# Optimization experiments

Hardware: AMD Instinct MI355X
Metric: run time of the kernel (lower is better)

Reference implementation:

```python
import jax, jax.numpy as jnp
import numpy as np

N_NODES = 100000
N_EDGES = 3200000
IN_FEATS = 512
HIDDEN = 64
N_CLASSES = 32


def setup_inputs() -> dict:
    key = jax.random.key(0)
    k1, k2, k3, k4 = jax.random.split(key, 4)
    x = jax.random.normal(k1, (N_NODES, IN_FEATS), dtype=jnp.float32)
    edge_index = jax.random.randint(k2, (2, N_EDGES), 0, N_NODES, dtype=jnp.int64)
    # Glorot-ish init for weights
    W1 = jax.random.normal(k3, (IN_FEATS, HIDDEN), dtype=jnp.float32) / np.sqrt(IN_FEATS)
    b1 = jnp.zeros((HIDDEN,), dtype=jnp.float32)
    W2 = jax.random.normal(k4, (HIDDEN, N_CLASSES), dtype=jnp.float32) / np.sqrt(HIDDEN)
    b2 = jnp.zeros((N_CLASSES,), dtype=jnp.float32)
    return {"x": x, "edge_index": edge_index, "W1": W1, "b1": b1, "W2": W2, "b2": b2}


def reference(x, edge_index, W1, b1, W2, b2):
    N = x.shape[0]
    # GCNConv default: add self-loops, unit edge weights (edge_attr is None for Cora)
    loop = jnp.arange(N, dtype=edge_index.dtype)
    src = jnp.concatenate([edge_index[0], loop])  # [E+N]
    dst = jnp.concatenate([edge_index[1], loop])  # [E+N]
    w = jnp.ones(src.shape[0], dtype=x.dtype)
    # symmetric normalization: deg^-1/2[src] * w * deg^-1/2[dst]
    deg = jax.ops.segment_sum(w, dst, num_segments=N)
    dinv = jnp.where(deg > 0, jax.lax.rsqrt(deg), 0.0)
    norm = dinv[src] * w * dinv[dst]  # [E+N]

    def gcn_layer(h, W, b):
        h = h @ W                              # transform first (out dim small)
        msg = h[src] * norm[:, None]           # gather + scale  [E+N, d_out]
        agg = jax.ops.segment_sum(msg, dst, num_segments=N)  # scatter-add
        return agg + b

    h = jax.nn.relu(gcn_layer(x, W1, b1))
    # F.dropout(training=self.training) -> identity in eval mode
    out = gcn_layer(h, W2, b2)
    return jax.nn.log_softmax(out, axis=1)
```

## Files before the change

### kernel.cpp

```cpp
#include <hip/hip_runtime.h>
#include <hip/hip_fp16.h>
#include <math.h>

constexpr int N_NODES = 100000;
constexpr int N_EDGES = 3200000;
constexpr int IN_F = 512;
constexpr int HID = 64;
constexpr int NCLS = 32;
constexpr int CAP = 80;
constexpr int SHIFT = 9;
constexpr int NB = 196;
constexpr int BCAPC = 16976;
constexpr int CHUNK = 8192;
constexpr int SENT = N_NODES;

constexpr int GEMM1_BLOCKS = (N_NODES + 63) / 64;
constexpr int PART_BLOCKS  = (N_EDGES + CHUNK - 1) / CHUNK;

typedef short short8 __attribute__((ext_vector_type(8)));
typedef float f32x4 __attribute__((ext_vector_type(4)));
typedef int intx4 __attribute__((ext_vector_type(4)));

__device__ __forceinline__ unsigned short f2bf(float f) {
    union { float f; unsigned int u; } v; v.f = f;
    unsigned int r = (v.u + 0x7fffu + ((v.u >> 16) & 1u)) >> 16;
    return (unsigned short)r;
}
__device__ __forceinline__ float bf2f(unsigned short h) {
    union { unsigned int u; float f; } v; v.u = ((unsigned int)h) << 16;
    return v.f;
}
__device__ __forceinline__ unsigned char f2e5(float f) {
    unsigned short u = __half_as_ushort(__float2half(f));
    return (unsigned char)((u + 0x7Fu + ((u >> 8) & 1u)) >> 8);
}
__device__ __forceinline__ float e52f(unsigned char b) {
    return __half2float(__ushort_as_half((unsigned short)((unsigned short)b << 8)));
}
__device__ __forceinline__ void gload16(const void* g, void* l) {
    __builtin_amdgcn_global_load_lds((const __attribute__((address_space(1))) unsigned int*)g,
                                     (__attribute__((address_space(3))) unsigned int*)l,
                                     16, 0, 0);
}

__global__ __launch_bounds__(256) void k_prep(const float* __restrict__ W1,
                                              unsigned short* __restrict__ W1T,
                                              unsigned char* __restrict__ h1s,
                                              unsigned char* __restrict__ h2s,
                                              int* __restrict__ gtail) {
    if (blockIdx.x == 128) {
        int t = threadIdx.x;
        if (t < HID)  h1s[(size_t)SENT * HID + t] = 0;
        if (t < NCLS) h2s[(size_t)SENT * NCLS + t] = 0;
        for (int i = t; i < NB * 16; i += 256) gtail[i] = 0;
        return;
    }
    int t = blockIdx.x * 256 + threadIdx.x;
    int k = t >> 6, c = t & 63;
    W1T[(size_t)c * IN_F + k] = f2bf(W1[(size_t)k * HID + c]);
}


__global__ __launch_bounds__(512) void k_part(const int* __restrict__ src,
                                              const int* __restrict__ dst,
                                              int* __restrict__ gtail,
                                              int* __restrict__ recs) {
    __shared__ alignas(16) char smem[47168];
    int* buf            = (int*)smem;
    unsigned char* bbuf = (unsigned char*)(smem + 32768);
    int* loc   = (int*)(smem + 40960);
    int* lh    = (int*)(smem + 43012);
    int* lbase = (int*)(smem + 45060);
    int* wsum  = (int*)(smem + 47108);
    const int tid = threadIdx.x;
    const int lane = tid & 63;
    const int wv = tid >> 6;
    const int c0 = blockIdx.x * CHUNK;
    const int cnum = min(CHUNK, N_EDGES - c0);
    lh[tid] = 0;
    __syncthreads();
    int dd[16], ss[16], rk[16];
    #pragma unroll
    for (int k = 0; k < 16; ++k) {
        int i = k * 512 + tid;
        if (i < cnum) {
            dd[k] = dst[c0 + i];
            ss[k] = src[c0 + i];
            rk[k] = atomicAdd(&lh[dd[k] >> SHIFT], 1);
        }
    }
    __syncthreads();
    int orig = lh[tid];
    int v = orig;
    #pragma unroll
    for (int off = 1; off < 64; off <<= 1) {
        int t = __shfl_up(v, off, 64);
        if (lane >= off) v += t;
    }
    if (lane == 63) wsum[wv] = v;
    __syncthreads();
    int pre = 0;
    #pragma unroll
    for (int k = 0; k < 8; ++k) if (k < wv) pre += wsum[k];
    int incl = v + pre;
    loc[tid] = incl - orig;
    if (tid < NB && orig > 0) lbase[tid] = atomicAdd(&gtail[tid * 16], orig);
    __syncthreads();
    #pragma unroll
    for (int k = 0; k < 16; ++k) {
        int i = k * 512 + tid;
        if (i < cnum) {
            int b = dd[k] >> SHIFT;
            int pos = loc[b] + rk[k];
            buf[pos] = ((dd[k] & 511) << 17) | ss[k];
            bbuf[pos] = (unsigned char)b;
        }
    }
    __syncthreads();
    for (int i = tid; i < cnum; i += 512) {
        int b = bbuf[i];
        int idx = lbase[b] + (i - loc[b]);
        if (idx < BCAPC) recs[(size_t)b * BCAPC + idx] = buf[i];
    }
}


__global__ __launch_bounds__(256) void k_gemm1(const float* __restrict__ x,
                                               const unsigned short* __restrict__ W1T,
                                               unsigned short* __restrict__ h1) {
    __shared__ alignas(16) char smem[24576];
    float* Xf = (float*)smem;
    unsigned short* Wf = (unsigned short*)(smem + 16384);
    const int tid = threadIdx.x;
    const int lane = tid & 63;
    const int row0 = blockIdx.x * 64;
    const int w = tid >> 6;
    const int r0l = (w >> 1) * 32;
    const int c0l = (w & 1) * 32;
    const int lrow = lane & 15;
    const int lkb = (lane >> 4) << 3;
    f32x4 acc00 = {0.f, 0.f, 0.f, 0.f}, acc01 = acc00, acc10 = acc00, acc11 = acc00;

    const int rowA0 = tid >> 3;
    const int rowA1 = 32 + (tid >> 3);
    const int gA = tid & 7;
    const float* srcX0 = x + (size_t)min(row0 + rowA0, N_NODES - 1) * IN_F + ((gA ^ (rowA0 & 7)) << 2);
    const float* srcX1 = x + (size_t)min(row0 + rowA1, N_NODES - 1) * IN_F + ((gA ^ (rowA1 & 7)) << 2);
    const int rowW = tid >> 2;
    const int gW = tid & 3;
    const unsigned short* srcW = W1T + (size_t)rowW * IN_F + ((gW ^ (rowW & 3)) << 3);
    char* ldsX0 = smem + (w << 10);
    char* ldsX1 = smem + 4096 + (w << 10);
    char* ldsW  = smem + 16384 + (w << 10);

    gload16(srcX0, ldsX0);
    gload16(srcX1, ldsX1);
    gload16(srcW,  ldsW);
    __syncthreads();

    const int RA = r0l + lrow, RA2 = RA + 16;
    const int RB = c0l + lrow, RB2 = RB + 16;
    const int qx = lkb >> 2;
    const int qw = lkb >> 3;
    const int sxA  = ((qx ^ (RA & 7)) << 2),  sxA_ = (((qx + 1) ^ (RA & 7)) << 2);
    const int sxB  = ((qx ^ (RA2 & 7)) << 2), sxB_ = (((qx + 1) ^ (RA2 & 7)) << 2);
    const int swB  = ((qw ^ (RB & 3)) << 3);
    const int swB2 = ((qw ^ (RB2 & 3)) << 3);

    #pragma unroll 2
    for (int s = 0; s < 16; ++s) {
        const int p = s & 1;
        if (s < 15) {
            gload16(srcX0 + (s + 1) * 32, ldsX0 + (p ^ 1) * 8192);
            gload16(srcX1 + (s + 1) * 32, ldsX1 + (p ^ 1) * 8192);
            gload16(srcW  + (s + 1) * 32, ldsW  + (p ^ 1) * 4096);
        }
        const float* xrA = Xf + p * 2048 + RA * 32;
        const float* xrB = Xf + p * 2048 + RA2 * 32;
        f32x4 va0 = *(const f32x4*)(xrA + sxA);
        f32x4 va1 = *(const f32x4*)(xrA + sxA_);
        f32x4 vb0 = *(const f32x4*)(xrB + sxB);
        f32x4 vb1 = *(const f32x4*)(xrB + sxB_);
        const unsigned short* wr = Wf + p * 2048;
        short8 b0 = *(const short8*)(wr + RB * 32 + swB);
        short8 b1 = *(const short8*)(wr + RB2 * 32 + swB2);
        short8 a0, a1;
        a0[0] = (short)f2bf(va0[0]); a0[1] = (short)f2bf(va0[1]);
        a0[2] = (short)f2bf(va0[2]); a0[3] = (short)f2bf(va0[3]);
        a0[4] = (short)f2bf(va1[0]); a0[5] = (short)f2bf(va1[1]);
        a0[6] = (short)f2bf(va1[2]); a0[7] = (short)f2bf(va1[3]);
        a1[0] = (short)f2bf(vb0[0]); a1[1] = (short)f2bf(vb0[1]);
        a1[2] = (short)f2bf(vb0[2]); a1[3] = (short)f2bf(vb0[3]);
        a1[4] = (short)f2bf(vb1[0]); a1[5] = (short)f2bf(vb1[1]);
        a1[6] = (short)f2bf(vb1[2]); a1[7] = (short)f2bf(vb1[3]);
        acc00 = __builtin_amdgcn_mfma_f32_16x16x32_bf16(a0, b0, acc00, 0, 0, 0);
        acc01 = __builtin_amdgcn_mfma_f32_16x16x32_bf16(a0, b1, acc01, 0, 0, 0);
        acc10 = __builtin_amdgcn_mfma_f32_16x16x32_bf16(a1, b0, acc10, 0, 0, 0);
        acc11 = __builtin_amdgcn_mfma_f32_16x16x32_bf16(a1, b1, acc11, 0, 0, 0);
        __syncthreads();
    }
    const int vr0 = row0 + r0l + ((lane >> 4) << 2);
    const int gc0 = c0l + (lane & 15);
    #pragma unroll
    for (int v = 0; v < 4; ++v) {
        int gr = vr0 + v;
        if (gr < N_NODES) {
            h1[(size_t)gr * HID + gc0]      = f2bf(acc00[v]);
            h1[(size_t)gr * HID + gc0 + 16] = f2bf(acc01[v]);
        }
        int gr2 = gr + 16;
        if (gr2 < N_NODES) {
            h1[(size_t)gr2 * HID + gc0]      = f2bf(acc10[v]);
            h1[(size_t)gr2 * HID + gc0 + 16] = f2bf(acc11[v]);
        }
    }
}


__global__ __launch_bounds__(1024) void k_phase2(const int* __restrict__ gtail,
                                                 const int* __restrict__ recs,
                                                 int* __restrict__ slots,
                                                 int* __restrict__ cnt,
                                                 float* __restrict__ dinv,
                                                 const unsigned short* __restrict__ h1,
                                                 unsigned char* __restrict__ h1s) {
    __shared__ int scnt[512];
    const int b = blockIdx.x;
    const int tid = threadIdx.x;
    if (tid < 512) scnt[tid] = 0;
    __syncthreads();
    int nrec = min(gtail[b * 16], BCAPC);
    const int* rb = recs + (size_t)b * BCAPC;
    for (int i = tid; i < nrec; i += 1024) {
        int r = rb[i];
        int ln = r >> 17;
        int s  = r & 0x1FFFF;
        int p = atomicAdd(&scnt[ln], 1);
        int node = (b << SHIFT) + ln;
        if (p < CAP) slots[(size_t)node * CAP + p] = s;
    }
    __syncthreads();
    if (tid < 512) {
        int node = (b << SHIFT) + tid;
        if (node < N_NODES) {
            int c = scnt[tid];
            cnt[node] = c;
            dinv[node] = rsqrtf(1.0f + (float)c);
            int c2 = min(c, CAP);
            int degp = (c2 + 15) & ~15;
            for (int p = c2; p < degp; ++p) slots[(size_t)node * CAP + p] = SENT;
        }
    }
    for (int idx = tid; idx < 512 * 8; idx += 1024) {
        int ln = idx >> 3, g = idx & 7;
        int node = (b << SHIFT) + ln;
        if (node >= N_NODES) continue;
        float dv = rsqrtf(1.0f + (float)scnt[ln]);
        const unsigned short* hr = h1 + (size_t)node * HID;
        unsigned char* hs = h1s + (size_t)node * HID;
        short8 hv = *reinterpret_cast<const short8*>(hr + g * 8);
        unsigned int lo = 0, hi = 0;
        #pragma unroll
        for (int e = 0; e < 4; ++e)
            lo |= (unsigned int)f2e5(bf2f((unsigned short)hv[e]) * dv) << (e * 8);
        #pragma unroll
        for (int e = 0; e < 4; ++e)
            hi |= (unsigned int)f2e5(bf2f((unsigned short)hv[4 + e]) * dv) << (e * 8);
        *reinterpret_cast<uint2*>(hs + g * 8) = make_uint2(lo, hi);
    }
}


__global__ __launch_bounds__(256) void k_gather1(const int* __restrict__ cnt,
                                                 const int* __restrict__ slots,
                                                 const float* __restrict__ dinv,
                                                 const unsigned char* __restrict__ h1s,
                                                 const float* __restrict__ b1,
                                                 const float* __restrict__ W2,
                                                 unsigned char* __restrict__ h2s) {
    __shared__ alignas(16) float hsh[4][64];
    const int lane = threadIdx.x & 63;
    const int wv = threadIdx.x >> 6;
    const int cls = lane & 31;
    const int half = lane >> 5;
    float w[32];
    #pragma unroll
    for (int j = 0; j < 32; ++j)
        w[j] = W2[(size_t)(half * 32 + j) * NCLS + cls];
    const float bb = b1[lane];
    const int nw = gridDim.x * 4;
    for (int n0 = blockIdx.x * 4 + wv; n0 < N_NODES; n0 += nw) {
        const int n = __builtin_amdgcn_readfirstlane(n0);
        float dn = dinv[n];
        int deg = min(cnt[n], CAP);
        int degp = (deg + 15) & ~15;
        size_t base = (size_t)n * CAP;
        float a0 = e52f(h1s[(((unsigned)n) << 6) + lane]);
        float a1 = 0.f, a2 = 0.f, a3 = 0.f, a4 = 0.f, a5 = 0.f, a6 = 0.f, a7 = 0.f;
        for (int j = 0; j < degp; j += 16) {
            intx4 sa = __builtin_nontemporal_load(reinterpret_cast<const intx4*>(&slots[base + j]));
            intx4 sb = __builtin_nontemporal_load(reinterpret_cast<const intx4*>(&slots[base + j + 4]));
            intx4 sc = __builtin_nontemporal_load(reinterpret_cast<const intx4*>(&slots[base + j + 8]));
            intx4 sd = __builtin_nontemporal_load(reinterpret_cast<const intx4*>(&slots[base + j + 12]));
            a0 += e52f(h1s[(((unsigned)sa.x) << 6) + lane]);
            a1 += e52f(h1s[(((unsigned)sa.y) << 6) + lane]);
            a2 += e52f(h1s[(((unsigned)sa.z) << 6) + lane]);
            a3 += e52f(h1s[(((unsigned)sa.w) << 6) + lane]);
            a4 += e52f(h1s[(((unsigned)sb.x) << 6) + lane]);
            a5 += e52f(h1s[(((unsigned)sb.y) << 6) + lane]);
            a6 += e52f(h1s[(((unsigned)sb.z) << 6) + lane]);
            a7 += e52f(h1s[(((unsigned)sb.w) << 6) + lane]);
            a0 += e52f(h1s[(((unsigned)sc.x) << 6) + lane]);
            a1 += e52f(h1s[(((unsigned)sc.y) << 6) + lane]);
            a2 += e52f(h1s[(((unsigned)sc.z) << 6) + lane]);
            a3 += e52f(h1s[(((unsigned)sc.w) << 6) + lane]);
            a4 += e52f(h1s[(((unsigned)sd.x) << 6) + lane]);
            a5 += e52f(h1s[(((unsigned)sd.y) << 6) + lane]);
            a6 += e52f(h1s[(((unsigned)sd.z) << 6) + lane]);
            a7 += e52f(h1s[(((unsigned)sd.w) << 6) + lane]);
        }
        float v = fmaf(((a0 + a1) + (a2 + a3)) + ((a4 + a5) + (a6 + a7)), dn, bb);
        v = fmaxf(v, 0.f);
        hsh[wv][lane] = v;
        float acc = 0.f;
        #pragma unroll
        for (int q = 0; q < 8; ++q) {
            f32x4 hv = *reinterpret_cast<const f32x4*>(&hsh[wv][half * 32 + q * 4]);
            acc = fmaf(hv.x, w[q * 4 + 0], acc);
            acc = fmaf(hv.y, w[q * 4 + 1], acc);
            acc = fmaf(hv.z, w[q * 4 + 2], acc);
            acc = fmaf(hv.w, w[q * 4 + 3], acc);
        }
        acc += __shfl_xor(acc, 32, 64);
        if (half == 0)
            h2s[(((unsigned)n) << 5) + cls] = f2e5(acc * dn);
    }
}


__global__ __launch_bounds__(256) void k_out(const int* __restrict__ cnt,
                                             const int* __restrict__ slots,
                                             const float* __restrict__ dinv,
                                             const unsigned char* __restrict__ h2s,
                                             const float* __restrict__ b2,
                                             float* __restrict__ out) {
    int wid = blockIdx.x * 4 + (threadIdx.x >> 6);
    int n = __builtin_amdgcn_readfirstlane(wid);
    if (n >= N_NODES) return;
    int lane = threadIdx.x & 63;
    int cls = lane & 31;
    int half = lane >> 5;
    float dn = dinv[n];
    int deg = min(cnt[n], CAP);
    int degp = (deg + 15) & ~15;
    size_t base = (size_t)n * CAP;
    float a0 = half ? 0.f : e52f(h2s[(((unsigned)n) << 5) + cls]);
    float a1 = 0.f, a2 = 0.f, a3 = 0.f;
    for (int j = 0; j < degp; j += 16) {
        intx4 s0 = __builtin_nontemporal_load(
            reinterpret_cast<const intx4*>(&slots[base + j + half * 8]));
        intx4 s1 = __builtin_nontemporal_load(
            reinterpret_cast<const intx4*>(&slots[base + j + half * 8 + 4]));
        a0 += e52f(h2s[(((unsigned)s0.x) << 5) + cls]);
        a1 += e52f(h2s[(((unsigned)s0.y) << 5) + cls]);
        a2 += e52f(h2s[(((unsigned)s0.z) << 5) + cls]);
        a3 += e52f(h2s[(((unsigned)s0.w) << 5) + cls]);
        a0 += e52f(h2s[(((unsigned)s1.x) << 5) + cls]);
        a1 += e52f(h2s[(((unsigned)s1.y) << 5) + cls]);
        a2 += e52f(h2s[(((unsigned)s1.z) << 5) + cls]);
        a3 += e52f(h2s[(((unsigned)s1.w) << 5) + cls]);
    }
    float acc = (a0 + a1) + (a2 + a3);
    acc += __shfl_xor(acc, 32, 64);
    float z = fmaf(acc, dn, b2[cls]);
    float mx = z;
    #pragma unroll
    for (int d = 16; d > 0; d >>= 1) mx = fmaxf(mx, __shfl_xor(mx, d, 32));
    float ex = expf(z - mx);
    float sm = ex;
    #pragma unroll
    for (int d = 16; d > 0; d >>= 1) sm += __shfl_xor(sm, d, 32);
    if (half == 0)
        out[(size_t)n * NCLS + cls] = z - mx - logf(sm);
}


extern "C" void kernel_launch(void* const* d_in, const int* in_sizes, int n_in,
                              void* d_out, int out_size, void* d_ws, size_t ws_size,
                              hipStream_t stream) {
    const float* x  = (const float*)d_in[0];
    const int*   ei = (const int*)d_in[1];
    const float* W1 = (const float*)d_in[2];
    const float* b1 = (const float*)d_in[3];
    const float* W2 = (const float*)d_in[4];
    const float* b2 = (const float*)d_in[5];
    float* out = (float*)d_out;
    char* ws = (char*)d_ws;

    const int* src = ei;
    const int* dst = ei + N_EDGES;

    int*   gtail = (int*)ws;
    int*   cnt   = (int*)(ws + 16384);
    float* dinv  = (float*)(ws + 416384);
    unsigned short* W1T = (unsigned short*)(ws + 816384);
    int*   slots = (int*)(ws + 881920);
    unsigned short* h1 = (unsigned short*)(ws + 32882048ull);
    unsigned char* h1s = (unsigned char*)(ws + 45682048ull);
    char*  recs_base   = ws + 52082176ull;
    int*   recs  = (int*)recs_base;
    unsigned char* h2s  = (unsigned char*)(ws + 65391360ull);

    k_prep<<<129, 256, 0, stream>>>(W1, W1T, h1s, h2s, gtail);
    k_part<<<PART_BLOCKS, 512, 0, stream>>>(src, dst, gtail, recs);
    k_gemm1<<<GEMM1_BLOCKS, 256, 0, stream>>>(x, W1T, h1);
    k_phase2<<<NB, 1024, 0, stream>>>(gtail, recs, slots, cnt, dinv, h1, h1s);
    k_gather1<<<1536, 256, 0, stream>>>(cnt, slots, dinv, h1s, b1, W2, h2s);
    k_out<<<(N_NODES + 3) / 4, 256, 0, stream>>>(cnt, slots, dinv, h2s, b2, out);
}
```

Before: 200.0 us.

## Deepen GEMM1 global-to-LDS pipeline to four stages with partial vmcnt waits

Replaces the double-buffered K loop in the first-layer GEMM with a four-buffer ring, prefetching three stages ahead. Each stage waits only on its own loads via explicit s_waitcnt vmcnt counts and uses a single barrier, instead of a full sync per iteration. The aim is to hide more global-memory latency on the bandwidth-heavy read of x. In exchange, LDS use doubles to 48KB per block, which may lower occupancy.

```diff
diff --git a/kernel.cpp b/kernel.cpp
--- a/kernel.cpp
+++ b/kernel.cpp
@@ -128,9 +128,9 @@
 __global__ __launch_bounds__(256) void k_gemm1(const float* __restrict__ x,
                                                const unsigned short* __restrict__ W1T,
                                                unsigned short* __restrict__ h1) {
-    __shared__ alignas(16) char smem[24576];
+    __shared__ alignas(16) char smem[49152];
     float* Xf = (float*)smem;
-    unsigned short* Wf = (unsigned short*)(smem + 16384);
+    unsigned short* Wf = (unsigned short*)(smem + 32768);
     const int tid = threadIdx.x;
     const int lane = tid & 63;
     const int row0 = blockIdx.x * 64;
@@ -151,12 +151,14 @@
     const unsigned short* srcW = W1T + (size_t)rowW * IN_F + ((gW ^ (rowW & 3)) << 3);
     char* ldsX0 = smem + (w << 10);
     char* ldsX1 = smem + 4096 + (w << 10);
-    char* ldsW  = smem + 16384 + (w << 10);
-
-    gload16(srcX0, ldsX0);
-    gload16(srcX1, ldsX1);
-    gload16(srcW,  ldsW);
-    __syncthreads();
+    char* ldsW  = smem + 32768 + (w << 10);
+
+    #pragma unroll
+    for (int s = 0; s < 3; ++s) {
+        gload16(srcX0 + s * 32, ldsX0 + s * 8192);
+        gload16(srcX1 + s * 32, ldsX1 + s * 8192);
+        gload16(srcW  + s * 32, ldsW  + s * 4096);
+    }
 
     const int RA = r0l + lrow, RA2 = RA + 16;
     const int RB = c0l + lrow, RB2 = RB + 16;
@@ -167,38 +169,54 @@
     const int swB  = ((qw ^ (RB & 3)) << 3);
     const int swB2 = ((qw ^ (RB2 & 3)) << 3);
 
-    #pragma unroll 2
-    for (int s = 0; s < 16; ++s) {
-        const int p = s & 1;
-        if (s < 15) {
-            gload16(srcX0 + (s + 1) * 32, ldsX0 + (p ^ 1) * 8192);
-            gload16(srcX1 + (s + 1) * 32, ldsX1 + (p ^ 1) * 8192);
-            gload16(srcW  + (s + 1) * 32, ldsW  + (p ^ 1) * 4096);
-        }
-        const float* xrA = Xf + p * 2048 + RA * 32;
-        const float* xrB = Xf + p * 2048 + RA2 * 32;
-        f32x4 va0 = *(const f32x4*)(xrA + sxA);
-        f32x4 va1 = *(const f32x4*)(xrA + sxA_);
-        f32x4 vb0 = *(const f32x4*)(xrB + sxB);
-        f32x4 vb1 = *(const f32x4*)(xrB + sxB_);
-        const unsigned short* wr = Wf + p * 2048;
-        short8 b0 = *(const short8*)(wr + RB * 32 + swB);
-        short8 b1 = *(const short8*)(wr + RB2 * 32 + swB2);
-        short8 a0, a1;
-        a0[0] = (short)f2bf(va0[0]); a0[1] = (short)f2bf(va0[1]);
-        a0[2] = (short)f2bf(va0[2]); a0[3] = (short)f2bf(va0[3]);
-        a0[4] = (short)f2bf(va1[0]); a0[5] = (short)f2bf(va1[1]);
-        a0[6] = (short)f2bf(va1[2]); a0[7] = (short)f2bf(va1[3]);
-        a1[0] = (short)f2bf(vb0[0]); a1[1] = (short)f2bf(vb0[1]);
-        a1[2] = (short)f2bf(vb0[2]); a1[3] = (short)f2bf(vb0[3]);
-        a1[4] = (short)f2bf(vb1[0]); a1[5] = (short)f2bf(vb1[1]);
-        a1[6] = (short)f2bf(vb1[2]); a1[7] = (short)f2bf(vb1[3]);
-        acc00 = __builtin_amdgcn_mfma_f32_16x16x32_bf16(a0, b0, acc00, 0, 0, 0);
-        acc01 = __builtin_amdgcn_mfma_f32_16x16x32_bf16(a0, b1, acc01, 0, 0, 0);
-        acc10 = __builtin_amdgcn_mfma_f32_16x16x32_bf16(a1, b0, acc10, 0, 0, 0);
-        acc11 = __builtin_amdgcn_mfma_f32_16x16x32_bf16(a1, b1, acc11, 0, 0, 0);
-        __syncthreads();
-    }
+#define GEMM_COMPUTE(S)                                                          \
+    {                                                                            \
+        const int b_ = (S) & 3;                                                  \
+        const float* xrA = Xf + b_ * 2048 + RA * 32;                             \
+        const float* xrB = Xf + b_ * 2048 + RA2 * 32;                            \
+        f32x4 va0 = *(const f32x4*)(xrA + sxA);                                  \
+        f32x4 va1 = *(const f32x4*)(xrA + sxA_);                                 \
+        f32x4 vb0 = *(const f32x4*)(xrB + sxB);                                  \
+        f32x4 vb1 = *(const f32x4*)(xrB + sxB_);                                 \
+        const unsigned short* wr = Wf + b_ * 2048;                               \
+        short8 b0 = *(const short8*)(wr + RB * 32 + swB);                        \
+        short8 b1 = *(const short8*)(wr + RB2 * 32 + swB2);                      \
+        short8 a0, a1;                                                           \
+        a0[0] = (short)f2bf(va0[0]); a0[1] = (short)f2bf(va0[1]);                \
+        a0[2] = (short)f2bf(va0[2]); a0[3] = (short)f2bf(va0[3]);                \
+        a0[4] = (short)f2bf(va1[0]); a0[5] = (short)f2bf(va1[1]);                \
+        a0[6] = (short)f2bf(va1[2]); a0[7] = (short)f2bf(va1[3]);                \
+        a1[0] = (short)f2bf(vb0[0]); a1[1] = (short)f2bf(vb0[1]);                \
+        a1[2] = (short)f2bf(vb0[2]); a1[3] = (short)f2bf(vb0[3]);                \
+        a1[4] = (short)f2bf(vb1[0]); a1[5] = (short)f2bf(vb1[1]);                \
+        a1[6] = (short)f2bf(vb1[2]); a1[7] = (short)f2bf(vb1[3]);                \
+        acc00 = __builtin_amdgcn_mfma_f32_16x16x32_bf16(a0, b0, acc00, 0, 0, 0); \
+        acc01 = __builtin_amdgcn_mfma_f32_16x16x32_bf16(a0, b1, acc01, 0, 0, 0); \
+        acc10 = __builtin_amdgcn_mfma_f32_16x16x32_bf16(a1, b0, acc10, 0, 0, 0); \
+        acc11 = __builtin_amdgcn_mfma_f32_16x16x32_bf16(a1, b1, acc11, 0, 0, 0); \
+    }
+
+    for (int s = 0; s < 14; ++s) {
+        asm volatile("s_waitcnt vmcnt(6)" ::: "memory");
+        __builtin_amdgcn_s_barrier();
+        __builtin_amdgcn_sched_barrier(0);
+        if (s < 13) {
+            gload16(srcX0 + (s + 3) * 32, ldsX0 + ((s + 3) & 3) * 8192);
+            gload16(srcX1 + (s + 3) * 32, ldsX1 + ((s + 3) & 3) * 8192);
+            gload16(srcW  + (s + 3) * 32, ldsW  + ((s + 3) & 3) * 4096);
+        }
+        GEMM_COMPUTE(s);
+    }
+    asm volatile("s_waitcnt vmcnt(3)" ::: "memory");
+    __builtin_amdgcn_s_barrier();
+    __builtin_amdgcn_sched_barrier(0);
+    GEMM_COMPUTE(14);
+    asm volatile("s_waitcnt vmcnt(0)" ::: "memory");
+    __builtin_amdgcn_s_barrier();
+    __builtin_amdgcn_sched_barrier(0);
+    GEMM_COMPUTE(15);
+#undef GEMM_COMPUTE
+
     const int vr0 = row0 + r0l + ((lane >> 4) << 2);
     const int gc0 = c0l + (lane & 15);
     #pragma unroll
```

Result: no change. 197.5 us (-1.3%).
